# Optimization experiments

Hardware: AMD Instinct MI355X
Metric: run time of the kernel (lower is better)

## Reference

```python
import jax, jax.numpy as jnp
import numpy as np

N_NODES = 50000
N_EDGES = 1600000
IN_DIM = 256
OUT_DIM = 32
HEADS = 4


def setup_inputs() -> dict:
    key = jax.random.key(0)
    k1, k2, k3, k4, k5, k6 = jax.random.split(key, 6)
    x = jax.random.normal(k1, (N_NODES, IN_DIM), dtype=jnp.float32)
    adj_indices = jax.random.randint(k2, (N_EDGES, 2), 0, N_NODES, dtype=jnp.int64)
    adj_weights = jax.random.uniform(k3, (N_EDGES,), dtype=jnp.float32)
    # Parameters (torch Linear weight layout: [out_features, in_features])
    W = jax.random.normal(k4, (OUT_DIM * HEADS, IN_DIM), dtype=jnp.float32) / np.sqrt(IN_DIM)
    a_src = jax.random.normal(k5, (HEADS, OUT_DIM), dtype=jnp.float32)
    a_dst = jax.random.normal(k6, (HEADS, OUT_DIM), dtype=jnp.float32)
    return {"x": x, "adj_indices": adj_indices, "adj_weights": adj_weights,
            "W": W, "a_src": a_src, "a_dst": a_dst}


def reference(x, adj_indices, adj_weights, W, a_src, a_dst):
    N = x.shape[0]
    H, D = a_src.shape
    h = (x @ W.T).reshape(N, H, D)                      # [N,H,D]
    src = adj_indices[:, 0]
    dst = adj_indices[:, 1]
    hs = h[src]                                         # [E,H,D]
    hd = h[dst]                                         # [E,H,D]
    e = (hs * a_src).sum(-1) + (hd * a_dst).sum(-1)     # [E,H]
    e = jnp.tanh(e) * adj_weights[:, None]
    # Numerically-stable per-destination-node segment softmax (vectorized
    # replacement of the per-node Python loop in the original).
    emax = jax.ops.segment_max(e, dst, num_segments=N)  # [N,H]
    emax = jnp.where(jnp.isfinite(emax), emax, jnp.float32(0.0))
    ex = jnp.exp(e - emax[dst])                         # [E,H]
    denom = jax.ops.segment_sum(ex, dst, num_segments=N)  # [N,H]
    alpha = ex / denom[dst]
    m = alpha[:, :, None] * hs                          # [E,H,D]
    out = jax.ops.segment_sum(m, dst, num_segments=N)   # [N,H,D]
    out = out.reshape(N, H * D)
    # dropout is identity in eval mode; torch nn.GELU() is exact (erf) GELU
    return jax.nn.gelu(out, approximate=False)
```

## Files before the change

kernel.cpp:

```cpp
#include <hip/hip_runtime.h>
#include <math.h>

#define IN_DIM 256
#define HD     128
#define HEADS  4
#define SC_ELEMS 1024

typedef unsigned int  uint;
typedef unsigned short ushort;

__device__ __forceinline__ ushort f2bf(float f) {
  uint b = __float_as_uint(f);
  return (ushort)((b + 0x7fffu + ((b >> 16) & 1u)) >> 16);
}

__global__ __launch_bounds__(256) void gemm_xwt(
    const float* __restrict__ x, const float* __restrict__ W,
    float* __restrict__ h, int n) {
  __shared__ float xs[32][68];
  __shared__ float ws[32][132];
  const int tid = threadIdx.x;
  const int n0  = blockIdx.x * 64;
  const int tx  = tid & 15;
  const int ty  = tid >> 4;

  float acc[4][8];
  #pragma unroll
  for (int i = 0; i < 4; ++i)
    #pragma unroll
    for (int j = 0; j < 8; ++j) acc[i][j] = 0.f;

  for (int k0 = 0; k0 < IN_DIM; k0 += 32) {
    #pragma unroll
    for (int l = 0; l < 2; ++l) {
      int lin = tid + l * 256;
      int row = lin >> 3;
      int c4  = lin & 7;
      int gr  = n0 + row;
      float4 v = make_float4(0.f, 0.f, 0.f, 0.f);
      if (gr < n) v = *(const float4*)&x[(size_t)gr * IN_DIM + k0 + c4 * 4];
      xs[c4 * 4 + 0][row] = v.x;
      xs[c4 * 4 + 1][row] = v.y;
      xs[c4 * 4 + 2][row] = v.z;
      xs[c4 * 4 + 3][row] = v.w;
    }
    #pragma unroll
    for (int l = 0; l < 4; ++l) {
      int lin = tid + l * 256;
      int row = lin >> 3;
      int c4  = lin & 7;
      float4 v = *(const float4*)&W[(size_t)row * IN_DIM + k0 + c4 * 4];
      ws[c4 * 4 + 0][row] = v.x;
      ws[c4 * 4 + 1][row] = v.y;
      ws[c4 * 4 + 2][row] = v.z;
      ws[c4 * 4 + 3][row] = v.w;
    }
    __syncthreads();
    #pragma unroll
    for (int k = 0; k < 32; ++k) {
      float4 a4 = *(const float4*)&xs[k][ty * 4];
      float4 b0 = *(const float4*)&ws[k][tx * 8];
      float4 b1 = *(const float4*)&ws[k][tx * 8 + 4];
      float av[4] = {a4.x, a4.y, a4.z, a4.w};
      float bv[8] = {b0.x, b0.y, b0.z, b0.w, b1.x, b1.y, b1.z, b1.w};
      #pragma unroll
      for (int i = 0; i < 4; ++i)
        #pragma unroll
        for (int j = 0; j < 8; ++j)
          acc[i][j] = fmaf(av[i], bv[j], acc[i][j]);
    }
    __syncthreads();
  }
  #pragma unroll
  for (int i = 0; i < 4; ++i) {
    int gr = n0 + ty * 4 + i;
    if (gr < n) {
      float4 v0 = make_float4(acc[i][0], acc[i][1], acc[i][2], acc[i][3]);
      float4 v1 = make_float4(acc[i][4], acc[i][5], acc[i][6], acc[i][7]);
      *(float4*)&h[(size_t)gr * HD + tx * 8]     = v0;
      *(float4*)&h[(size_t)gr * HD + tx * 8 + 4] = v1;
    }
  }
}

__global__ __launch_bounds__(256) void cast_h(
    const float* __restrict__ h, ushort* __restrict__ hb, int total4) {
  int i = blockIdx.x * 256 + threadIdx.x;
  if (i >= total4) return;
  float4 v = ((const float4*)h)[i];
  uint a = ((uint)f2bf(v.y) << 16) | f2bf(v.x);
  uint b = ((uint)f2bf(v.w) << 16) | f2bf(v.z);
  ((uint2*)hb)[i] = make_uint2(a, b);
}

__global__ __launch_bounds__(256) void attn_proj(
    const float* __restrict__ h, const float* __restrict__ a_src,
    const float* __restrict__ a_dst, float* __restrict__ s,
    float* __restrict__ t, int n) {
  int gid = blockIdx.x * 256 + threadIdx.x;
  if (gid >= n * HEADS) return;
  int node = gid >> 2, head = gid & 3;
  const float4* hp = (const float4*)&h[(size_t)node * HD + head * 32];
  const float4* as = (const float4*)&a_src[head * 32];
  const float4* ad = (const float4*)&a_dst[head * 32];
  float ss = 0.f, tt = 0.f;
  #pragma unroll
  for (int i = 0; i < 8; ++i) {
    float4 hv = hp[i], av = as[i], dv = ad[i];
    ss += hv.x * av.x + hv.y * av.y + hv.z * av.z + hv.w * av.w;
    tt += hv.x * dv.x + hv.y * dv.y + hv.z * dv.z + hv.w * dv.w;
  }
  s[gid] = ss;
  t[gid] = tt;
}

__global__ __launch_bounds__(256) void hist_deg(
    const int* __restrict__ adj, int* __restrict__ deg, int E) {
  int e = blockIdx.x * 256 + threadIdx.x;
  if (e < E) {
    int dst = adj[2 * (size_t)e + 1];
    atomicAdd(&deg[dst], 1);
  }
}

__global__ __launch_bounds__(256) void scan_blocks(
    const int* __restrict__ deg, int* __restrict__ bsum, int n) {
  __shared__ int sm[256];
  int tid  = threadIdx.x;
  int base = blockIdx.x * SC_ELEMS + tid * 4;
  int s = 0;
  if (base + 3 < n) {
    int4 v = *(const int4*)&deg[base];
    s = v.x + v.y + v.z + v.w;
  } else {
    #pragma unroll
    for (int i = 0; i < 4; ++i) if (base + i < n) s += deg[base + i];
  }
  sm[tid] = s;
  __syncthreads();
  #pragma unroll
  for (int off = 128; off > 0; off >>= 1) {
    if (tid < off) sm[tid] += sm[tid + off];
    __syncthreads();
  }
  if (tid == 0) bsum[blockIdx.x] = sm[0];
}

__global__ __launch_bounds__(64) void scan_bsums(
    int* __restrict__ bsum, int nb, int* __restrict__ rowptr, int n) {
  int lane = threadIdx.x;
  int v = (lane < nb) ? bsum[lane] : 0;
  #pragma unroll
  for (int off = 1; off < 64; off <<= 1) {
    int u = __shfl_up(v, off, 64);
    if (lane >= off) v += u;
  }
  int excl = __shfl_up(v, 1, 64);
  if (lane == 0) excl = 0;
  if (lane < nb) bsum[lane] = excl;
  if (lane == 63) rowptr[n] = v;
}

__global__ __launch_bounds__(256) void scan_write(
    const int* __restrict__ deg, const int* __restrict__ bsum,
    int* __restrict__ rowptr, int* __restrict__ cursor, int n) {
  __shared__ int sm[256];
  int tid  = threadIdx.x;
  int base = blockIdx.x * SC_ELEMS + tid * 4;
  int4 v = make_int4(0, 0, 0, 0);
  if (base + 3 < n) {
    v = *(const int4*)&deg[base];
  } else {
    if (base + 0 < n) v.x = deg[base + 0];
    if (base + 1 < n) v.y = deg[base + 1];
    if (base + 2 < n) v.z = deg[base + 2];
    if (base + 3 < n) v.w = deg[base + 3];
  }
  int tsum = v.x + v.y + v.z + v.w;
  sm[tid] = tsum;
  __syncthreads();
  #pragma unroll
  for (int off = 1; off < 256; off <<= 1) {
    int a   = sm[tid];
    int add = (tid >= off) ? sm[tid - off] : 0;
    __syncthreads();
    sm[tid] = a + add;
    __syncthreads();
  }
  int run = ((tid == 0) ? 0 : sm[tid - 1]) + bsum[blockIdx.x];
  int r0 = run, r1 = r0 + v.x, r2 = r1 + v.y, r3 = r2 + v.z;
  if (base + 0 < n) { rowptr[base + 0] = r0; cursor[base + 0] = r0; }
  if (base + 1 < n) { rowptr[base + 1] = r1; cursor[base + 1] = r1; }
  if (base + 2 < n) { rowptr[base + 2] = r2; cursor[base + 2] = r2; }
  if (base + 3 < n) { rowptr[base + 3] = r3; cursor[base + 3] = r3; }
}

__global__ __launch_bounds__(256) void scatter_edges(
    const int* __restrict__ adj, const float* __restrict__ wts,
    const float* __restrict__ s, const float* __restrict__ t,
    int* __restrict__ cursor, int* __restrict__ src_sorted,
    float* __restrict__ e_sorted, int E) {
  int e = blockIdx.x * 256 + threadIdx.x;
  if (e >= E) return;
  int src = adj[2 * (size_t)e];
  int dst = adj[2 * (size_t)e + 1];
  float w = wts[e];
  float4 sv = *(const float4*)&s[(size_t)src * 4];
  float4 tv = *(const float4*)&t[(size_t)dst * 4];
  float4 ev;
  ev.x = tanhf(sv.x + tv.x) * w;
  ev.y = tanhf(sv.y + tv.y) * w;
  ev.z = tanhf(sv.z + tv.z) * w;
  ev.w = tanhf(sv.w + tv.w) * w;
  int pos = atomicAdd(&cursor[dst], 1);
  src_sorted[pos] = src;
  *(float4*)&e_sorted[(size_t)pos * 4] = ev;
}

__global__ __launch_bounds__(256) void node_max(
    const float* __restrict__ evals, const int* __restrict__ rowptr,
    float* __restrict__ emax, int n4) {
  int gid = blockIdx.x * 256 + threadIdx.x;
  if (gid >= n4) return;
  int node = gid >> 2, head = gid & 3;
  int beg = rowptr[node], end = rowptr[node + 1];
  float m = -INFINITY;
  #pragma unroll 4
  for (int k = beg; k < end; ++k)
    m = fmaxf(m, evals[(size_t)k * 4 + head]);
  emax[gid] = m;
}

__global__ __launch_bounds__(256) void aggregate(
    const ushort* __restrict__ hb, const int* __restrict__ rowptr,
    const int* __restrict__ srcs, const float* __restrict__ evals,
    const float* __restrict__ emax, float* __restrict__ out, int n) {
  int node = blockIdx.x * 4 + (threadIdx.x >> 6);
  int lane = threadIdx.x & 63;
  if (node >= n) return;
  int head = lane >> 4;
  int beg = rowptr[node], end = rowptr[node + 1];
  float m = emax[node * 4 + head];

  float l = 0.f, accx = 0.f, accy = 0.f;
  #pragma unroll 2
  for (int k = beg; k < end; ++k) {
    int   srcC = srcs[k];
    float eC   = evals[(size_t)k * 4 + head];
    uint  hv   = *(const uint*)&hb[(size_t)srcC * HD + lane * 2];
    float p  = __expf(eC - m);
    float hx = __uint_as_float(hv << 16);
    float hy = __uint_as_float(hv & 0xffff0000u);
    l += p;
    accx = fmaf(p, hx, accx);
    accy = fmaf(p, hy, accy);
  }

  float2 o = make_float2(0.f, 0.f);
  if (end > beg) { float r = 1.f / l; o.x = accx * r; o.y = accy * r; }
  o.x = 0.5f * o.x * (1.f + erff(o.x * 0.70710678118654752f));
  o.y = 0.5f * o.y * (1.f + erff(o.y * 0.70710678118654752f));
  *(float2*)&out[(size_t)node * HD + lane * 2] = o;
}

__global__ void ws_too_small(float* out, int n) {
  int i = blockIdx.x * 256 + threadIdx.x;
  if (i < n) out[i] = -12345.0f;
}

extern "C" void kernel_launch(void* const* d_in, const int* in_sizes, int n_in,
                              void* d_out, int out_size, void* d_ws, size_t ws_size,
                              hipStream_t stream) {
  const float* x     = (const float*)d_in[0];
  const int*   adj   = (const int*)d_in[1];
  const float* wts   = (const float*)d_in[2];
  const float* W     = (const float*)d_in[3];
  const float* a_src = (const float*)d_in[4];
  const float* a_dst = (const float*)d_in[5];
  const int N = in_sizes[0] / IN_DIM;
  const int E = in_sizes[1] / 2;
  float* out = (float*)d_out;
  (void)n_in;

  const int NB = (N + SC_ELEMS - 1) / SC_ELEMS;

  size_t off = 0;
  auto take = [&](size_t bytes) -> char* {
    char* p = (char*)d_ws + off;
    off += (bytes + 255) & ~(size_t)255;
    return p;
  };
  float* h          = (float*)take((size_t)N * HD * 4);
  float* s          = (float*)take((size_t)N * HEADS * 4);
  float* t          = (float*)take((size_t)N * HEADS * 4);
  int*   deg        = (int*)take((size_t)N * 4);
  int*   rowptr     = (int*)take((size_t)(N + 1) * 4);
  int*   cursor     = (int*)take((size_t)N * 4);
  int*   bsum       = (int*)take((size_t)64 * 4);
  int*   src_sorted = (int*)take((size_t)E * 4);
  float* e_sorted   = (float*)take((size_t)E * 4 * 4);
  float* emax       = (float*)take((size_t)N * HEADS * 4);
  size_t base_off = off;

  ushort* hb = (ushort*)take((size_t)N * HD * 2);
  if (off > ws_size) {
    hb = (ushort*)d_in[0];
    off = base_off;
  }
  if (off > ws_size) {
    ws_too_small<<<(out_size + 255) / 256, 256, 0, stream>>>(out, out_size);
    return;
  }

  hipMemsetAsync(deg, 0, (size_t)N * 4, stream);

  gemm_xwt<<<(N + 63) / 64, 256, 0, stream>>>(x, W, h, N);
  cast_h<<<(N * HD / 4 + 255) / 256, 256, 0, stream>>>(h, hb, N * HD / 4);
  attn_proj<<<(N * HEADS + 255) / 256, 256, 0, stream>>>(h, a_src, a_dst, s, t, N);
  hist_deg<<<(E + 255) / 256, 256, 0, stream>>>(adj, deg, E);
  scan_blocks<<<NB, 256, 0, stream>>>(deg, bsum, N);
  scan_bsums<<<1, 64, 0, stream>>>(bsum, NB, rowptr, N);
  scan_write<<<NB, 256, 0, stream>>>(deg, bsum, rowptr, cursor, N);
  scatter_edges<<<(E + 255) / 256, 256, 0, stream>>>(adj, wts, s, t, cursor,
                                                     src_sorted, e_sorted, E);
  node_max<<<(N * HEADS + 255) / 256, 256, 0, stream>>>(e_sorted, rowptr, emax,
                                                        N * HEADS);
  aggregate<<<(N + 3) / 4, 256, 0, stream>>>(hb, rowptr, src_sorted, e_sorted,
                                             emax, out, N);
}
```

Before: 447.7 us.

## Drop per-node max pass and pack src with bf16 edge scores

Removes the node_max kernel and the max subtraction in the softmax. Because the scores are tanh times a weight in [0,1), they are bounded in [-1,1], so exp cannot overflow. Source index and four bf16-rounded edge scores are packed into one int4 per sorted edge, so aggregate reads one 16-byte record instead of separate index and float4 arrays. This saves one kernel launch and one full pass over the sorted edge scores. In exchange, the scores lose precision to bf16 and the unused int4 slot adds padding.

```diff
diff --git a/kernel.cpp b/kernel.cpp
--- a/kernel.cpp
+++ b/kernel.cpp
@@ -198,8 +198,7 @@
 __global__ __launch_bounds__(256) void scatter_edges(
     const int* __restrict__ adj, const float* __restrict__ wts,
     const float* __restrict__ s, const float* __restrict__ t,
-    int* __restrict__ cursor, int* __restrict__ src_sorted,
-    float* __restrict__ e_sorted, int E) {
+    int* __restrict__ cursor, int4* __restrict__ epack, int E) {
   int e = blockIdx.x * 256 + threadIdx.x;
   if (e >= E) return;
   int src = adj[2 * (size_t)e];
@@ -207,48 +206,37 @@
   float w = wts[e];
   float4 sv = *(const float4*)&s[(size_t)src * 4];
   float4 tv = *(const float4*)&t[(size_t)dst * 4];
-  float4 ev;
-  ev.x = tanhf(sv.x + tv.x) * w;
-  ev.y = tanhf(sv.y + tv.y) * w;
-  ev.z = tanhf(sv.z + tv.z) * w;
-  ev.w = tanhf(sv.w + tv.w) * w;
+  float e0 = tanhf(sv.x + tv.x) * w;
+  float e1 = tanhf(sv.y + tv.y) * w;
+  float e2 = tanhf(sv.z + tv.z) * w;
+  float e3 = tanhf(sv.w + tv.w) * w;
+  int4 pk;
+  pk.x = src;
+  pk.y = (int)(((uint)f2bf(e1) << 16) | f2bf(e0));
+  pk.z = (int)(((uint)f2bf(e3) << 16) | f2bf(e2));
+  pk.w = 0;
   int pos = atomicAdd(&cursor[dst], 1);
-  src_sorted[pos] = src;
-  *(float4*)&e_sorted[(size_t)pos * 4] = ev;
-}
-
-__global__ __launch_bounds__(256) void node_max(
-    const float* __restrict__ evals, const int* __restrict__ rowptr,
-    float* __restrict__ emax, int n4) {
-  int gid = blockIdx.x * 256 + threadIdx.x;
-  if (gid >= n4) return;
-  int node = gid >> 2, head = gid & 3;
-  int beg = rowptr[node], end = rowptr[node + 1];
-  float m = -INFINITY;
-  #pragma unroll 4
-  for (int k = beg; k < end; ++k)
-    m = fmaxf(m, evals[(size_t)k * 4 + head]);
-  emax[gid] = m;
+  epack[pos] = pk;
 }
 
 __global__ __launch_bounds__(256) void aggregate(
     const ushort* __restrict__ hb, const int* __restrict__ rowptr,
-    const int* __restrict__ srcs, const float* __restrict__ evals,
-    const float* __restrict__ emax, float* __restrict__ out, int n) {
+    const int4* __restrict__ epack, float* __restrict__ out, int n) {
   int node = blockIdx.x * 4 + (threadIdx.x >> 6);
   int lane = threadIdx.x & 63;
   if (node >= n) return;
   int head = lane >> 4;
   int beg = rowptr[node], end = rowptr[node + 1];
-  float m = emax[node * 4 + head];
 
   float l = 0.f, accx = 0.f, accy = 0.f;
   #pragma unroll 2
   for (int k = beg; k < end; ++k) {
-    int   srcC = srcs[k];
-    float eC   = evals[(size_t)k * 4 + head];
-    uint  hv   = *(const uint*)&hb[(size_t)srcC * HD + lane * 2];
-    float p  = __expf(eC - m);
+    int4 pk = epack[k];
+    uint pe   = (head & 2) ? (uint)pk.z : (uint)pk.y;
+    uint bits = (head & 1) ? (pe & 0xffff0000u) : (pe << 16);
+    float eC  = __uint_as_float(bits);
+    uint  hv  = *(const uint*)&hb[(size_t)pk.x * HD + lane * 2];
+    float p  = __expf(eC);
     float hx = __uint_as_float(hv << 16);
     float hy = __uint_as_float(hv & 0xffff0000u);
     l += p;
@@ -290,16 +278,14 @@
     off += (bytes + 255) & ~(size_t)255;
     return p;
   };
-  float* h          = (float*)take((size_t)N * HD * 4);
-  float* s          = (float*)take((size_t)N * HEADS * 4);
-  float* t          = (float*)take((size_t)N * HEADS * 4);
-  int*   deg        = (int*)take((size_t)N * 4);
-  int*   rowptr     = (int*)take((size_t)(N + 1) * 4);
-  int*   cursor     = (int*)take((size_t)N * 4);
-  int*   bsum       = (int*)take((size_t)64 * 4);
-  int*   src_sorted = (int*)take((size_t)E * 4);
-  float* e_sorted   = (float*)take((size_t)E * 4 * 4);
-  float* emax       = (float*)take((size_t)N * HEADS * 4);
+  float* h      = (float*)take((size_t)N * HD * 4);
+  float* s      = (float*)take((size_t)N * HEADS * 4);
+  float* t      = (float*)take((size_t)N * HEADS * 4);
+  int*   deg    = (int*)take((size_t)N * 4);
+  int*   rowptr = (int*)take((size_t)(N + 1) * 4);
+  int*   cursor = (int*)take((size_t)N * 4);
+  int*   bsum   = (int*)take((size_t)64 * 4);
+  int4*  epack  = (int4*)take((size_t)E * 16);
   size_t base_off = off;
 
   ushort* hb = (ushort*)take((size_t)N * HD * 2);
@@ -322,9 +308,6 @@
   scan_bsums<<<1, 64, 0, stream>>>(bsum, NB, rowptr, N);
   scan_write<<<NB, 256, 0, stream>>>(deg, bsum, rowptr, cursor, N);
   scatter_edges<<<(E + 255) / 256, 256, 0, stream>>>(adj, wts, s, t, cursor,
-                                                     src_sorted, e_sorted, E);
-  node_max<<<(N * HEADS + 255) / 256, 256, 0, stream>>>(e_sorted, rowptr, emax,
-                                                        N * HEADS);
-  aggregate<<<(N + 3) / 4, 256, 0, stream>>>(hb, rowptr, src_sorted, e_sorted,
-                                             emax, out, N);
-}
+                                                     epack, E);
+  aggregate<<<(N + 3) / 4, 256, 0, stream>>>(hb, rowptr, epack, out, N);
+}
```

Measured after the change: 422.2 us. -5.7%, faster.
